# Optimization experiments

Hardware: AMD Instinct MI355X
Metric: run time of the kernel (lower is better)

## Reference

```python
import jax, jax.numpy as jnp
import numpy as np

B, T, H, N = 1, 256, 32, 128
HN = H * N
KVH = 8
KV_DIM = KVH * N
KV_REPEAT = HN // KV_DIM
ROPE_THETA = 10000.0
EPS = 1e-6
NTK_ALPHA = 10.0
YARN_MAX = 4096.0
LORA_W, LORA_A, LORA_V, LORA_G = 64, 64, 32, 128
LAYER_ID = 1


def t5_rmsnorm(x, w):
    xf = x.astype(jnp.float32)
    var = jnp.mean(xf * xf, axis=-1, keepdims=True)
    return (w * (xf * jax.lax.rsqrt(var + EPS))).astype(x.dtype)


def rotate_half(x):
    h = x.shape[-1] // 2
    return jnp.concatenate([-x[..., h:], x[..., :h]], axis=-1)


def rope_cache(cache_pos, seq_len, rotary_dim):
    # YaRN-style mix of short/long inv_freq, per compute_rope_cache_range
    half = rotary_dim // 2
    fs = jnp.arange(half, dtype=jnp.float32)
    inv_short = 1.0 / ROPE_THETA ** (fs / half)
    inv_long = 1.0 / (ROPE_THETA * NTK_ALPHA ** (fs / half))
    pos = cache_pos.astype(jnp.float32) + jnp.arange(seq_len, dtype=jnp.float32)[None, :]  # [B,T]
    mix = jnp.clip(pos / YARN_MAX, 0.0, 1.0)[..., None]
    freqs = (1.0 - mix) * (pos[..., None] * inv_short) + mix * (pos[..., None] * inv_long)
    emb = jnp.concatenate([freqs, freqs], axis=-1)  # [B,T,rotary_dim]
    return jnp.cos(emb), jnp.sin(emb)


def _forward(x_in, v_first, state, cache_position, w0, w1, w2, a0, a1, a2, v0, v1, v2, g1, g2,
             r_k, R_, K_, V_, O_, R_bias, K_bias, V_bias, ln_r, ln_k, ln1, ln2):
    x = t5_rmsnorm(x_in, ln1)  # [B,T,HN]
    # float path of fpx_matmul: x @ W.T (+ bias), i.e. the dequantized math
    r = x @ R_.T + R_bias
    k = x @ K_.T + K_bias
    v = x @ V_.T + V_bias
    r = t5_rmsnorm(r.reshape(B, T, H, N), ln_r)      # [B,T,H,N]
    k = t5_rmsnorm(k.reshape(B, T, KVH, N), ln_k)    # [B,T,KVH,N]
    cos, sin = rope_cache(cache_position, T, N)      # [B,T,N]
    cos_, sin_ = cos[:, :, None, :], sin[:, :, None, :]
    r = r * cos_ + rotate_half(r) * sin_
    k = k * cos_ + rotate_half(k) * sin_
    # decay lora: w = -softplus(-(tanh(x@w1)@w2 + w0)) - 0.5
    w = jnp.tanh(x @ w1) @ w2 + w0
    w = -jax.nn.softplus(-w) - 0.5
    # GQA repeat_kv: each kv head repeated KV_REPEAT times contiguously
    v = v.reshape(B, T, KVH, N)
    k = jnp.repeat(k, KV_REPEAT, axis=2).reshape(B, T, HN)
    v = jnp.repeat(v, KV_REPEAT, axis=2).reshape(B, T, HN)
    a = jax.nn.sigmoid((x @ a1) @ a2 + a0)
    g = jax.nn.sigmoid(x @ g1) @ g2
    k4 = k.reshape(B, T, H, N)
    kk = (k4 / jnp.maximum(jnp.linalg.norm(k4, axis=-1, keepdims=True), 1e-12)).reshape(B, T, HN)
    k = k * (1.0 - w + a)
    aa = -kk
    bb = kk * a
    if LAYER_ID == 0:
        v_first = v
    else:
        gate = jax.nn.sigmoid((x @ v1) @ v2 + v0)
        v = v + (v_first - v) * gate
    w = -jnp.exp(w.astype(jnp.float32))  # log-decay for the recurrence

    def to_tm(t):  # [B,T,HN] or [B,T,H,N] -> time-major [T,B,H,N]
        return jnp.moveaxis(t.reshape(B, T, H, N), 1, 0)

    rt, wt, kt, vt, at, bt = map(to_tm, (r, w, k, v, aa, bb))

    def step(S, inp):
        # RWKV-7: S = S*diag(exp(w)) + S @ (a b^T) + v k^T ; out = S @ r
        r_t, w_t, k_t, v_t, a_t, b_t = inp
        sa = jnp.einsum('bhij,bhj->bhi', S, a_t)
        S = S * jnp.exp(w_t)[:, :, None, :] + sa[..., None] * b_t[:, :, None, :] + v_t[..., None] * k_t[:, :, None, :]
        return S, jnp.einsum('bhij,bhj->bhi', S, r_t)

    S_final, outs = jax.lax.scan(step, state.astype(jnp.float32), (rt, wt, kt, vt, at, bt))
    xx = jnp.moveaxis(outs, 0, 1).reshape(B, T, HN) * (float(N) ** -0.5)
    bonus = jnp.sum(r.reshape(B, T, H, N) * k.reshape(B, T, H, N) * r_k, axis=-1, keepdims=True) * v.reshape(B, T, H, N)
    xx = xx.astype(r.dtype) + bonus.reshape(B, T, HN)
    x_res = x_in + (xx * g) @ O_.T
    out = t5_rmsnorm(x_res, ln2)
    return out, x[:, -1], S_final, v_first, x_res


def setup_inputs() -> dict:
    key = jax.random.key(0)
    ks = iter(jax.random.split(key, 32))
    rn = lambda *s: jax.random.normal(next(ks), s, dtype=jnp.float32)
    wt = lambda *s: rn(*s) * 0.02
    return dict(
        x_in=rn(B, T, HN),
        v_first=rn(B, T, HN),
        state=jnp.zeros((B, H, N, N), jnp.float32),
        cache_position=jnp.zeros((B, 1), jnp.int32),
        w0=wt(HN), w1=wt(HN, LORA_W), w2=wt(LORA_W, HN),
        a0=wt(HN), a1=wt(HN, LORA_A), a2=wt(LORA_A, HN),
        v0=wt(HN), v1=wt(HN, LORA_V), v2=wt(LORA_V, HN),
        g1=wt(HN, LORA_G), g2=wt(LORA_G, HN),
        r_k=wt(H, N),
        R_=wt(HN, HN), K_=wt(KV_DIM, HN), V_=wt(KV_DIM, HN), O_=wt(HN, HN),
        R_bias=wt(HN), K_bias=wt(KV_DIM), V_bias=wt(KV_DIM),
        ln_r=jnp.ones((N,), jnp.float32), ln_k=jnp.ones((N,), jnp.float32),
        ln1=jnp.ones((HN,), jnp.float32), ln2=jnp.ones((HN,), jnp.float32),
    )


def reference(x_in, v_first, state, cache_position, w0, w1, w2, a0, a1, a2, v0, v1, v2, g1, g2,
              r_k, R_, K_, V_, O_, R_bias, K_bias, V_bias, ln_r, ln_k, ln1, ln2):
    return _forward(x_in, v_first, state, cache_position, w0, w1, w2, a0, a1, a2, v0, v1, v2,
                    g1, g2, r_k, R_, K_, V_, O_, R_bias, K_bias, V_bias, ln_r, ln_k, ln1, ln2)
```

## Files before the change

kernel.cpp:

```cpp
#include <hip/hip_runtime.h>
#include <cstdint>
#include <cstddef>

#define T_ 256
#define HN_ 4096
#define H_ 32
#define N_ 128
#define SR_ 6464

typedef __attribute__((ext_vector_type(8))) short short8;
typedef __attribute__((ext_vector_type(4))) float f32x4;

__device__ __forceinline__ short f2bf(float f) {
    uint32_t u = __builtin_bit_cast(uint32_t, f);
    u = (u + 0x7fffu + ((u >> 16) & 1u)) >> 16;
    return (short)u;
}
__device__ __forceinline__ short f2bfc(float f) {
    return (short)((__builtin_bit_cast(uint32_t, f) + 0x8000u) >> 16);
}
__device__ __forceinline__ short8 cvt8r(float4 lo, float4 hi) {
    short8 v;
    v[0] = f2bfc(lo.x); v[1] = f2bfc(lo.y); v[2] = f2bfc(lo.z); v[3] = f2bfc(lo.w);
    v[4] = f2bfc(hi.x); v[5] = f2bfc(hi.y); v[6] = f2bfc(hi.z); v[7] = f2bfc(hi.w);
    return v;
}
__device__ __forceinline__ f32x4 mfma16(short8 a, short8 b, f32x4 c) {
    return __builtin_amdgcn_mfma_f32_16x16x32_bf16(a, b, c, 0, 0, 0);
}
__device__ __forceinline__ float sigm(float x) { return 1.f / (1.f + expf(-x)); }
__device__ __forceinline__ float splus(float x) { return (x > 20.f) ? x : log1pf(expf(x)); }

__device__ __forceinline__ float bf1(ushort u) {
    return __builtin_bit_cast(float, (uint32_t)u << 16);
}
__device__ __forceinline__ void gload_lds16(const void* g, void* l) {
    __builtin_amdgcn_global_load_lds(
        (const __attribute__((address_space(1))) void*)g,
        (__attribute__((address_space(3))) void*)l, 16, 0, 0);
}

template <int CTRL>
__device__ __forceinline__ float dpp_add(float v) {
    int p = __builtin_amdgcn_mov_dpp(__builtin_bit_cast(int, v), CTRL, 0xF, 0xF, true);
    return v + __builtin_bit_cast(float, p);
}
__device__ __forceinline__ float reduce64(float v) {
    v = dpp_add<0xB1>(v);
    v = dpp_add<0x4E>(v);
    v = dpp_add<0x124>(v);
    v = dpp_add<0x128>(v);
    v = dpp_add<0x142>(v);
    v = dpp_add<0x143>(v);
    int r = __builtin_amdgcn_readlane(__builtin_bit_cast(int, v), 63);
    return __builtin_bit_cast(float, r);
}

__device__ __forceinline__ void gemm_core(
    const ushort* __restrict__ A, const float* __restrict__ Brow,
    int kbeg, float* LB, f32x4 acc[2][2]) {
    const int tid = threadIdx.x, wid = tid >> 6, l = tid & 63;
    const int ar = l & 15, ak = (l >> 4) * 8;
    const int mBase = wid * 32;

    const int p1 = tid, p2 = tid + 512;
    const int r1 = p1 >> 5, c1 = (p1 & 31) ^ (r1 & 7);
    const int r2 = p2 >> 5, c2 = (p2 & 31) ^ (r2 & 7);
    const float* sb1 = Brow + (size_t)r1 * 4096 + kbeg + c1 * 4;
    const float* sb2 = Brow + (size_t)r2 * 4096 + kbeg + c2 * 4;
    float* d1 = LB + wid * 256;
    float* d2 = LB + 2048 + wid * 256;

    const ushort* pa0 = A + (size_t)(mBase + ar) * 4096 + kbeg + ak;
    const ushort* pa1 = pa0 + (size_t)16 * 4096;

    const int rb0 = ar * 128, rb1 = (16 + ar) * 128;
    const int sx = ar & 7;
    const int cb = (l >> 4) * 2;

    short8 Ae[8], Ao[8];

#define STAGEB(s, rb) { \
    gload_lds16(sb1 + (size_t)(s) * 128, d1 + (rb) * 4096); \
    gload_lds16(sb2 + (size_t)(s) * 128, d2 + (rb) * 4096); }

#define LA(B_, s) { \
    B_[0] = *(const short8*)(pa0 + (size_t)(s) * 128);      \
    B_[1] = *(const short8*)(pa1 + (size_t)(s) * 128);      \
    B_[2] = *(const short8*)(pa0 + (size_t)(s) * 128 + 32); \
    B_[3] = *(const short8*)(pa1 + (size_t)(s) * 128 + 32); \
    B_[4] = *(const short8*)(pa0 + (size_t)(s) * 128 + 64); \
    B_[5] = *(const short8*)(pa1 + (size_t)(s) * 128 + 64); \
    B_[6] = *(const short8*)(pa0 + (size_t)(s) * 128 + 96); \
    B_[7] = *(const short8*)(pa1 + (size_t)(s) * 128 + 96); }

#define CKK(kk, B_, Lb_) { \
    const int cc = (kk) * 8 + cb; \
    float4 l0 = *(const float4*)(Lb_ + rb0 + ((cc ^ sx) * 4)); \
    float4 h0 = *(const float4*)(Lb_ + rb0 + (((cc + 1) ^ sx) * 4)); \
    float4 l1 = *(const float4*)(Lb_ + rb1 + ((cc ^ sx) * 4)); \
    float4 h1 = *(const float4*)(Lb_ + rb1 + (((cc + 1) ^ sx) * 4)); \
    short8 b0 = cvt8r(l0, h0), b1 = cvt8r(l1, h1); \
    acc[0][0] = mfma16(B_[2 * (kk)], b0, acc[0][0]); \
    acc[0][1] = mfma16(B_[2 * (kk)], b1, acc[0][1]); \
    acc[1][0] = mfma16(B_[2 * (kk) + 1], b0, acc[1][0]); \
    acc[1][1] = mfma16(B_[2 * (kk) + 1], b1, acc[1][1]); }

#define COMPUTE(rb, B_) { const float* Lb_ = LB + (rb) * 4096; \
    CKK(0, B_, Lb_) CKK(1, B_, Lb_) CKK(2, B_, Lb_) CKK(3, B_, Lb_) }

    STAGEB(0, 0)
    LA(Ae, 0)
    STAGEB(1, 1)

    for (int su = 0; su < 4; su++) {
        const int s0 = su * 2, s1 = su * 2 + 1;
        LA(Ao, (s0 + 1 < 8) ? s0 + 1 : 7)
        STAGEB((s0 + 2 < 8) ? s0 + 2 : 7, (s0 + 2) % 3)
        asm volatile("s_waitcnt vmcnt(12)" ::: "memory");
        __builtin_amdgcn_s_barrier();
        __builtin_amdgcn_sched_barrier(0);
        COMPUTE(s0 % 3, Ae)
        __builtin_amdgcn_s_barrier();

        LA(Ae, (s1 + 1 < 8) ? s1 + 1 : 7)
        STAGEB((s1 + 2 < 8) ? s1 + 2 : 7, (s1 + 2) % 3)
        asm volatile("s_waitcnt vmcnt(12)" ::: "memory");
        __builtin_amdgcn_s_barrier();
        __builtin_amdgcn_sched_barrier(0);
        COMPUTE(s1 % 3, Ao)
        __builtin_amdgcn_s_barrier();
    }
    asm volatile("s_waitcnt vmcnt(0)" ::: "memory");
#undef STAGEB
#undef LA
#undef CKK
#undef COMPUTE
}

__global__ __launch_bounds__(256) void rmsnorm_k(const float* __restrict__ in,
                                                 const float* __restrict__ w,
                                                 float* __restrict__ outF,
                                                 ushort* __restrict__ outB,
                                                 float* __restrict__ lastrow) {
    int t = blockIdx.x, tid = threadIdx.x;
    const float4* in4 = (const float4*)(in + (size_t)t * HN_);
    const float4* w4 = (const float4*)w;
    float4 v[4]; float ss = 0.f;
#pragma unroll
    for (int q = 0; q < 4; q++) {
        v[q] = in4[q * 256 + tid];
        ss += v[q].x * v[q].x + v[q].y * v[q].y + v[q].z * v[q].z + v[q].w * v[q].w;
    }
#pragma unroll
    for (int o = 32; o; o >>= 1) ss += __shfl_down(ss, o);
    __shared__ float red[4];
    if ((tid & 63) == 0) red[tid >> 6] = ss;
    __syncthreads();
    float tot = red[0] + red[1] + red[2] + red[3];
    float sc = rsqrtf(tot * (1.f / HN_) + 1e-6f);
#pragma unroll
    for (int q = 0; q < 4; q++) {
        float4 wv = w4[q * 256 + tid];
        float4 r;
        r.x = wv.x * v[q].x * sc; r.y = wv.y * v[q].y * sc;
        r.z = wv.z * v[q].z * sc; r.w = wv.w * v[q].w * sc;
        int idx = q * 256 + tid;
        if (outF) ((float4*)(outF + (size_t)t * HN_))[idx] = r;
        if (outB) {
            ushort4 b;
            b.x = (ushort)f2bf(r.x); b.y = (ushort)f2bf(r.y);
            b.z = (ushort)f2bf(r.z); b.w = (ushort)f2bf(r.w);
            ((ushort4*)(outB + (size_t)t * HN_))[idx] = b;
        }
        if (lastrow && t == T_ - 1) ((float4*)lastrow)[idx] = r;
    }
}

__global__ __launch_bounds__(512, 2) void gemm_rkvt(
    const ushort* __restrict__ A,
    const float* __restrict__ Rw, const float* __restrict__ Kw,
    const float* __restrict__ Vw, const float* __restrict__ WT,
    float* __restrict__ COMB) {
    __shared__ __align__(16) float LB[12288];
    const int tid = threadIdx.x, wid = tid >> 6, l = tid & 63;
    const int mBase = wid * 32;
    const int nB = blockIdx.x * 32;
    const int kbeg = blockIdx.y * 1024;

    const float* Bp; int brow;
    if (nB < 4096)      { Bp = Rw; brow = nB; }
    else if (nB < 5120) { Bp = Kw; brow = nB - 4096; }
    else if (nB < 6144) { Bp = Vw; brow = nB - 5120; }
    else                { Bp = WT; brow = nB - 6144; }

    f32x4 acc[2][2];
#pragma unroll
    for (int i = 0; i < 2; i++)
#pragma unroll
        for (int j = 0; j < 2; j++) acc[i][j] = f32x4{0.f, 0.f, 0.f, 0.f};

    gemm_core(A, Bp + (size_t)brow * 4096, kbeg, LB, acc);

    const int rl = (l >> 4) * 4, cl = l & 15;
#pragma unroll
    for (int mf = 0; mf < 2; mf++)
#pragma unroll
        for (int nf = 0; nf < 2; nf++)
#pragma unroll
            for (int e = 0; e < 4; e++)
                unsafeAtomicAdd(&COMB[(size_t)(mBase + mf * 16 + rl + e) * SR_ + nB + nf * 16 + cl],
                                acc[mf][nf][e]);
}

__global__ __launch_bounds__(512, 2) void gemm_o(
    const ushort* __restrict__ A,
    const float* __restrict__ B,
    float* __restrict__ C) {
    __shared__ __align__(16) float LB[12288];
    const int tid = threadIdx.x, wid = tid >> 6, l = tid & 63;
    const int mBase = wid * 32;
    const int nB = blockIdx.x * 32;
    const int kbeg = blockIdx.y * 1024;

    f32x4 acc[2][2];
#pragma unroll
    for (int i = 0; i < 2; i++)
#pragma unroll
        for (int j = 0; j < 2; j++) acc[i][j] = f32x4{0.f, 0.f, 0.f, 0.f};

    gemm_core(A, B + (size_t)nB * 4096, kbeg, LB, acc);

    const int rl = (l >> 4) * 4, cl = l & 15;
#pragma unroll
    for (int mf = 0; mf < 2; mf++)
#pragma unroll
        for (int nf = 0; nf < 2; nf++)
#pragma unroll
            for (int e = 0; e < 4; e++)
                unsafeAtomicAdd(&C[(size_t)(mBase + mf * 16 + rl + e) * 4096 + nB + nf * 16 + cl],
                                acc[mf][nf][e]);
}

__global__ __launch_bounds__(512) void gemm_s2(
    const ushort* __restrict__ TCB,
    const float* __restrict__ w2, const float* __restrict__ a2,
    const float* __restrict__ v2, const float* __restrict__ g2,
    const float* __restrict__ w0, const float* __restrict__ a0,
    const float* __restrict__ v0,
    float* __restrict__ WPRE, float* __restrict__ APRE,
    float* __restrict__ VGPRE, float* __restrict__ GARR) {
    const int z = blockIdx.y;
    int Aoff, K; const float* B; const float* bias; float* out;
    if (z == 0)      { Aoff = 0;   K = 64;  B = w2; bias = w0;      out = WPRE; }
    else if (z == 1) { Aoff = 64;  K = 64;  B = a2; bias = a0;      out = APRE; }
    else if (z == 2) { Aoff = 128; K = 32;  B = v2; bias = v0;      out = VGPRE; }
    else             { Aoff = 160; K = 128; B = g2; bias = nullptr; out = GARR; }

    const int tid = threadIdx.x, wid = tid >> 6, l = tid & 63;
    const int ar = l & 15, ak = (l >> 4) * 8;
    const int mBase = wid * 32;
    const int nB = blockIdx.x * 32;

    f32x4 acc[2][2];
#pragma unroll
    for (int i = 0; i < 2; i++)
#pragma unroll
        for (int j = 0; j < 2; j++) acc[i][j] = f32x4{0.f, 0.f, 0.f, 0.f};

    for (int k0 = 0; k0 < K; k0 += 32) {
        const ushort* pA = TCB + (size_t)(mBase + ar) * 320 + Aoff + k0 + ak;
        short8 av0 = *(const short8*)pA;
        short8 av1 = *(const short8*)(pA + (size_t)16 * 320);
        short8 bv0, bv1;
#pragma unroll
        for (int e = 0; e < 8; e++) {
            bv0[e] = f2bfc(B[(size_t)(k0 + ak + e) * 4096 + nB + ar]);
            bv1[e] = f2bfc(B[(size_t)(k0 + ak + e) * 4096 + nB + 16 + ar]);
        }
        acc[0][0] = mfma16(av0, bv0, acc[0][0]);
        acc[0][1] = mfma16(av0, bv1, acc[0][1]);
        acc[1][0] = mfma16(av1, bv0, acc[1][0]);
        acc[1][1] = mfma16(av1, bv1, acc[1][1]);
    }
    const int rl = (l >> 4) * 4, cl = l & 15;
#pragma unroll
    for (int mf = 0; mf < 2; mf++)
#pragma unroll
        for (int nf = 0; nf < 2; nf++) {
            int col = nB + nf * 16 + cl;
            float bv = bias ? bias[col] : 0.f;
#pragma unroll
            for (int e = 0; e < 4; e++)
                out[(size_t)(mBase + mf * 16 + rl + e) * 4096 + col] = acc[mf][nf][e] + bv;
        }
}

__global__ __launch_bounds__(256) void wcat2_k(const float* __restrict__ w1p,
                                               const float* __restrict__ a1p,
                                               const float* __restrict__ v1p,
                                               const float* __restrict__ g1p,
                                               float* __restrict__ WT) {
    const int kb = blockIdx.x * 64, tile = blockIdx.y;
    const float* src; int ldw, jo, nb, W;
    if (tile == 0)      { src = w1p; ldw = 64;  jo = 0;  nb = 0;   W = 64; }
    else if (tile == 1) { src = a1p; ldw = 64;  jo = 0;  nb = 64;  W = 64; }
    else if (tile == 2) { src = v1p; ldw = 32;  jo = 0;  nb = 128; W = 32; }
    else if (tile == 3) { src = g1p; ldw = 128; jo = 0;  nb = 160; W = 64; }
    else                { src = g1p; ldw = 128; jo = 64; nb = 224; W = 64; }
    __shared__ float lds[64][65];
    const int ti = threadIdx.x & 63, wi = threadIdx.x >> 6;
    if (ti < W)
        for (int i = wi; i < 64; i += 4)
            lds[i][ti] = src[(size_t)(kb + i) * ldw + jo + ti];
    __syncthreads();
    for (int i2 = wi; i2 < W; i2 += 4)
        WT[(size_t)(nb + i2) * 4096 + kb + ti] = lds[ti][i2];
}

__global__ __launch_bounds__(256) void init_comb_k(const float* __restrict__ Rb,
                                                   const float* __restrict__ Kb,
                                                   const float* __restrict__ Vb,
                                                   float* __restrict__ COMB) {
    int t = blockIdx.x;
    for (int c = threadIdx.x; c < SR_; c += 256) {
        float b = (c < 4096) ? Rb[c] : (c < 5120) ? Kb[c - 4096]
                : (c < 6144) ? Vb[c - 5120] : 0.f;
        COMB[(size_t)t * SR_ + c] = b;
    }
}

__global__ __launch_bounds__(256) void act_k(const float* __restrict__ COMB,
                                             ushort* __restrict__ TCB) {
    int idx = blockIdx.x * 256 + threadIdx.x;
    if (idx >= 256 * 288) return;
    int t = idx / 288, c = idx % 288;
    float v = COMB[(size_t)t * SR_ + 6144 + c];
    if (c < 64) v = tanhf(v);
    else if (c >= 160) v = sigm(v);
    TCB[t * 320 + c] = (ushort)f2bf(v);
}

__global__ __launch_bounds__(256) void prep_k(
    const float* __restrict__ COMB, const float* __restrict__ wpre,
    const float* __restrict__ apre, const float* __restrict__ vgpre,
    const float* __restrict__ vfirst, const float* __restrict__ garr,
    const float* __restrict__ rkg, const int* __restrict__ cpos,
    const float* __restrict__ lnr, const float* __restrict__ lnk,
    ushort* __restrict__ SFB) {
    const int tp = blockIdx.x, hg = blockIdx.y;
    const int tid = threadIdx.x;
    const int w = tid >> 6, lane = tid & 63;
    const int t0 = tp * 2, t1 = t0 + 1;

    float e = (float)lane * (1.f / 64.f);
    float inv_s = exp2f(-13.287712379549449f * e);
    float inv_l = exp2f(-13.287712379549449f - 3.321928094887362f * e);
    float base = (float)cpos[0];
    float pos0 = base + (float)t0, pos1 = base + (float)t1;
    float mix0 = fminf(fmaxf(pos0 * (1.f / 4096.f), 0.f), 1.f);
    float mix1 = fminf(fmaxf(pos1 * (1.f / 4096.f), 0.f), 1.f);
    float fr0 = pos0 * ((1.f - mix0) * inv_s + mix0 * inv_l);
    float fr1 = pos1 * ((1.f - mix1) * inv_s + mix1 * inv_l);
    float cA = cosf(fr0), sA = sinf(fr0);
    float cB = cosf(fr1), sB = sinf(fr1);

    float lr0 = lnr[lane], lr1 = lnr[lane + 64];
    float lk0 = lnk[lane], lk1 = lnk[lane + 64];

    for (int hb = hg * 4; hb < hg * 4 + 4; hb++) {
        int h = hb * 4 + w;
        int kv = h >> 2;
        float rk0 = rkg[h * 128 + lane], rk1 = rkg[h * 128 + 64 + lane];

        auto STEPQ = [&](int t, float cc, float ss,
                         float& Rr0, float& Rr1, float& Kf0, float& Kf1,
                         float& Aa0, float& Aa1, float& Bb0, float& Bb1,
                         float& Dd0, float& Dd1, float& Vv0, float& Vv1,
                         float& Gg0, float& Gg1) {
            size_t tS = (size_t)t * SR_;
            float r0 = COMB[tS + h * 128 + lane];
            float r1 = COMB[tS + h * 128 + 64 + lane];
            float sm = reduce64(r0 * r0 + r1 * r1);
            float sc = rsqrtf(sm * (1.f / 128.f) + 1e-6f);
            float rn0 = lr0 * r0 * sc, rn1 = lr1 * r1 * sc;
            Rr0 = rn0 * cc - rn1 * ss; Rr1 = rn1 * cc + rn0 * ss;
            float k0 = COMB[tS + 4096 + kv * 128 + lane];
            float k1 = COMB[tS + 4096 + kv * 128 + 64 + lane];
            float ks = reduce64(k0 * k0 + k1 * k1);
            float ksc = rsqrtf(ks * (1.f / 128.f) + 1e-6f);
            float kn0 = lk0 * k0 * ksc, kn1 = lk1 * k1 * ksc;
            float kr0 = kn0 * cc - kn1 * ss, kr1 = kn1 * cc + kn0 * ss;
            float nr = reduce64(kr0 * kr0 + kr1 * kr1);
            float inv = 1.f / fmaxf(sqrtf(nr), 1e-12f);
            float kk0 = kr0 * inv, kk1 = kr1 * inv;
            int ch0 = h * 128 + lane, ch1 = ch0 + 64;
            size_t tb = (size_t)t * HN_;
            float wv0 = -splus(-wpre[tb + ch0]) - 0.5f;
            float wv1 = -splus(-wpre[tb + ch1]) - 0.5f;
            Dd0 = expf(-expf(wv0)); Dd1 = expf(-expf(wv1));
            float av0 = sigm(apre[tb + ch0]);
            float av1 = sigm(apre[tb + ch1]);
            float vg0 = sigm(vgpre[tb + ch0]);
            float vg1 = sigm(vgpre[tb + ch1]);
            float vr0 = COMB[tS + 5120 + kv * 128 + lane];
            float vr1 = COMB[tS + 5120 + kv * 128 + 64 + lane];
            Vv0 = vr0 + (vfirst[tb + ch0] - vr0) * vg0;
            Vv1 = vr1 + (vfirst[tb + ch1] - vr1) * vg1;
            Kf0 = kr0 * (1.f - wv0 + av0); Kf1 = kr1 * (1.f - wv1 + av1);
            Aa0 = -kk0; Aa1 = -kk1;
            Bb0 = kk0 * av0; Bb1 = kk1 * av1;
            Gg0 = garr[tb + ch0]; Gg1 = garr[tb + ch1];
        };

        float r00, r01, k00, k01, a00, a01, b00, b01, d00, d01, v00, v01, g00, g01;
        float r10, r11, k10, k11, a10, a11, b10, b11, d10, d11, v10, v11, g10, g11;
        STEPQ(t0, cA, sA, r00, r01, k00, k01, a00, a01, b00, b01, d00, d01, v00, v01, g00, g01);
        STEPQ(t1, cB, sB, r10, r11, k10, k11, a10, a11, b10, b11, d10, d11, v10, v11, g10, g11);

        float* rf = (float*)(SFB + ((size_t)h * 128 + tp) * 3072);
        rf[0    + lane] = a00;        rf[0    + 64 + lane] = a01;
        rf[128  + lane] = d00 * a10;  rf[128  + 64 + lane] = d01 * a11;
        rf[256  + lane] = d00 * r00;  rf[256  + 64 + lane] = d01 * r01;
        rf[384  + lane] = r10;        rf[384  + 64 + lane] = r11;
        rf[512  + lane] = d00 * d10;  rf[512  + 64 + lane] = d01 * d11;
        rf[640  + lane] = b00 * d10;  rf[640  + 64 + lane] = b01 * d11;
        rf[768  + lane] = k00 * d10;  rf[768  + 64 + lane] = k01 * d11;
        rf[896  + lane] = b10;        rf[896  + 64 + lane] = b11;
        rf[1024 + lane] = k10;        rf[1024 + 64 + lane] = k11;
        ushort* us = (ushort*)rf;
        us[2304 + lane] = (ushort)f2bf(v00); us[2304 + 64 + lane] = (ushort)f2bf(v01);
        us[2432 + lane] = (ushort)f2bf(v10); us[2432 + 64 + lane] = (ushort)f2bf(v11);
        us[2560 + lane] = (ushort)f2bf(g00); us[2560 + 64 + lane] = (ushort)f2bf(g01);
        us[2688 + lane] = (ushort)f2bf(g10); us[2688 + 64 + lane] = (ushort)f2bf(g11);

        float C1  = reduce64(b00 * a10 + b01 * a11);
        float C2  = reduce64(k00 * a10 + k01 * a11);
        float C3  = reduce64(b00 * r00 + b01 * r01);
        float C4  = reduce64(k00 * r00 + k01 * r01);
        float BD0 = reduce64(r00 * k00 * rk0 + r01 * k01 * rk1);
        float BD1 = reduce64(r10 * k10 * rk0 + r11 * k11 * rk1);
        if (lane == 0) {
            rf[1408] = C1; rf[1409] = C2; rf[1410] = C3;
            rf[1411] = C4; rf[1412] = BD0; rf[1413] = BD1;
        }
    }
}

#define SDP_ 5
#define SNBP_ 6
__global__ __launch_bounds__(256) void scan_k(
    const float* __restrict__ state_in,
    const ushort* __restrict__ SFB,
    ushort* __restrict__ yb, float* __restrict__ Sout,
    ushort* __restrict__ dummy) {
    const int h = blockIdx.x, sp = blockIdx.y;
    const int tid = threadIdx.x;
    const int wv = tid >> 6, ln = tid & 63;
    const int i = sp * 4 + wv;
    const int j0 = ln * 2;

    float S0, S1;
    {
        float2 s2 = *(const float2*)(state_in + ((size_t)h * 128 + i) * 128 + j0);
        S0 = s2.x; S1 = s2.y;
    }

    __shared__ __align__(16) ushort lds_s[SNBP_][3072];
    const ushort* hbase = SFB + (size_t)h * 128 * 3072;

    auto STAGE = [&](int buf, int tp) {
        if (wv < 3) {
            const ushort* src = hbase + (size_t)(tp & 127) * 3072 + wv * 1024 + ln * 8;
            gload_lds16(src,       &lds_s[buf][wv * 1024]);
            gload_lds16(src + 512, &lds_s[buf][wv * 1024 + 512]);
        }
    };

#pragma unroll
    for (int d = 0; d < SDP_; d++) STAGE(d, d);

    float pend_y0 = 0.f, pend_y1 = 0.f;
    float r1c0 = 0.f, r1c1 = 0.f, bd1c = 0.f, vi1c = 0.f, gi1c = 0.f;
    for (int Io = 0; Io < 132; Io += 6) {
#pragma unroll
        for (int u = 0; u < 6; u++) {
            const int I = Io + u;
            if (I >= 128) break;
            const int bc = u;
            const int bs = (u + SDP_) % 6;

            if (wv < 3) {
                if (I < SDP_) asm volatile("s_waitcnt vmcnt(8)" ::: "memory");
                else          asm volatile("s_waitcnt vmcnt(16)" ::: "memory");
            }
            __builtin_amdgcn_s_barrier();
            __builtin_amdgcn_sched_barrier(0);
            asm volatile("" ::: "memory");

            if (ln == 0) {
                ushort* p0 = (I >= 1) ? (yb + (size_t)(2 * I - 2) * HN_ + h * 128 + i)
                                      : (dummy + tid);
                *p0 = (ushort)f2bf(pend_y0);
                ushort* p1 = (I >= 2) ? (yb + (size_t)(2 * I - 3) * HN_ + h * 128 + i)
                                      : (dummy + 256 + tid);
                *p1 = (ushort)f2bf(pend_y1);
            }

            STAGE(bs, I + SDP_);

            const ushort* L = lds_s[bc];
            const float* Lf = (const float*)L;
            float2 A0 = *(const float2*)(Lf + 0    + j0);
            float2 WA = *(const float2*)(Lf + 128  + j0);
            float2 WR = *(const float2*)(Lf + 256  + j0);
            float2 R1 = *(const float2*)(Lf + 384  + j0);
            float2 W2 = *(const float2*)(Lf + 512  + j0);
            float2 BW = *(const float2*)(Lf + 640  + j0);
            float2 KW = *(const float2*)(Lf + 768  + j0);
            float2 B1 = *(const float2*)(Lf + 896  + j0);
            float2 K1 = *(const float2*)(Lf + 1024 + j0);
            float vi0 = bf1(L[2304 + i]);
            float vi1 = bf1(L[2432 + i]);
            float gi0 = bf1(L[2560 + i]);
            float gi1 = bf1(L[2688 + i]);
            const float* Sc = Lf + 1408;
            float c1 = Sc[0], c2 = Sc[1], c3 = Sc[2], c4 = Sc[3];
            float bd0 = Sc[4], bd1 = Sc[5];

            float up = fmaf(S0, A0.x, S1 * A0.y);
            float pp = fmaf(S0, WA.x, S1 * WA.y);
            float yp = fmaf(S0, WR.x, S1 * WR.y);
            float op = fmaf(S0, r1c0, S1 * r1c1);
            float u_   = reduce64(up);
            float p_   = reduce64(pp);
            float yb0  = reduce64(yp);
            float od1  = reduce64(op);

            pend_y1 = fmaf(od1, 0.08838834764831845f, bd1c * vi1c) * gi1c;

            float sa0 = u_;
            float sa1 = fmaf(sa0, c1, fmaf(vi0, c2, p_));
            float od0 = fmaf(sa0, c3, fmaf(vi0, c4, yb0));
            pend_y0 = fmaf(od0, 0.08838834764831845f, bd0 * vi0) * gi0;

            S0 = fmaf(sa0, BW.x, S0 * W2.x);
            S0 = fmaf(vi0, KW.x, S0);
            S0 = fmaf(sa1, B1.x, S0);
            S0 = fmaf(vi1, K1.x, S0);
            S1 = fmaf(sa0, BW.y, S1 * W2.y);
            S1 = fmaf(vi0, KW.y, S1);
            S1 = fmaf(sa1, B1.y, S1);
            S1 = fmaf(vi1, K1.y, S1);

            r1c0 = R1.x; r1c1 = R1.y;
            bd1c = bd1; vi1c = vi1; gi1c = gi1;
        }
    }

    {
        float op = fmaf(S0, r1c0, S1 * r1c1);
        float od1 = reduce64(op);
        float cp1 = fmaf(od1, 0.08838834764831845f, bd1c * vi1c) * gi1c;
        if (ln == 0) {
            yb[(size_t)255 * HN_ + h * 128 + i] = (ushort)f2bf(cp1);
            yb[(size_t)254 * HN_ + h * 128 + i] = (ushort)f2bf(pend_y0);
            yb[(size_t)253 * HN_ + h * 128 + i] = (ushort)f2bf(pend_y1);
        }
    }

    float* pS = Sout + ((size_t)h * 128 + i) * 128 + j0;
    *(float2*)pS = make_float2(S0, S1);
}

extern "C" void kernel_launch(void* const* d_in, const int* in_sizes, int n_in,
                              void* d_out, int out_size, void* d_ws, size_t ws_size,
                              hipStream_t stream) {
    const float* x_in   = (const float*)d_in[0];
    const float* vfirst = (const float*)d_in[1];
    const float* state  = (const float*)d_in[2];
    const int*   cpos   = (const int*)d_in[3];
    const float* w0 = (const float*)d_in[4];
    const float* w1 = (const float*)d_in[5];
    const float* w2 = (const float*)d_in[6];
    const float* a0 = (const float*)d_in[7];
    const float* a1 = (const float*)d_in[8];
    const float* a2 = (const float*)d_in[9];
    const float* v0 = (const float*)d_in[10];
    const float* v1 = (const float*)d_in[11];
    const float* v2 = (const float*)d_in[12];
    const float* g1 = (const float*)d_in[13];
    const float* g2 = (const float*)d_in[14];
    const float* r_k = (const float*)d_in[15];
    const float* R_ = (const float*)d_in[16];
    const float* K_ = (const float*)d_in[17];
    const float* V_ = (const float*)d_in[18];
    const float* O_ = (const float*)d_in[19];
    const float* Rb = (const float*)d_in[20];
    const float* Kb = (const float*)d_in[21];
    const float* Vb = (const float*)d_in[22];
    const float* ln_r = (const float*)d_in[23];
    const float* ln_k = (const float*)d_in[24];
    const float* ln1 = (const float*)d_in[25];
    const float* ln2 = (const float*)d_in[26];

    float* ws = (float*)d_ws;
    constexpr size_t OFF_XB   = 0;
    constexpr size_t OFF_COMB = 524288;
    constexpr size_t OFF_WT   = 2179072;
    constexpr size_t OFF_TCB  = 3489792;
    constexpr size_t OFF_WPRE = 3530752;
    constexpr size_t OFF_APRE = 4579328;
    constexpr size_t OFF_VGPRE= 5627904;
    constexpr size_t OFF_G    = 6676480;
    constexpr size_t OFF_SF   = 7757824;
    constexpr size_t OFF_DUM  = 14049280;
    constexpr size_t OFF_YB   = OFF_XB;

    ushort* XB  = (ushort*)(ws + OFF_XB);
    float* COMB = ws + OFF_COMB;
    float* WT   = ws + OFF_WT;
    ushort* TCB = (ushort*)(ws + OFF_TCB);
    float* WPRE = ws + OFF_WPRE;
    float* APRE = ws + OFF_APRE;
    float* VGPRE= ws + OFF_VGPRE;
    float* GARR = ws + OFF_G;
    ushort* SFB = (ushort*)(ws + OFF_SF);
    ushort* DUM = (ushort*)(ws + OFF_DUM);
    ushort* YB  = (ushort*)(ws + OFF_YB);

    float* out = (float*)d_out;
    float* out0  = out;
    float* xlast = out + 1048576;
    float* Sfin  = out + 1052672;
    float* vfout = out + 1576960;
    float* xres  = out + 2625536;

    hipMemcpyAsync(vfout, vfirst, (size_t)1048576 * 4, hipMemcpyDeviceToDevice, stream);
    hipMemcpyAsync(xres, x_in, (size_t)1048576 * 4, hipMemcpyDeviceToDevice, stream);

    rmsnorm_k<<<T_, 256, 0, stream>>>(x_in, ln1, nullptr, XB, xlast);

    wcat2_k<<<dim3(64, 5), 256, 0, stream>>>(w1, a1, v1, g1, WT);
    hipMemsetAsync(WT + (size_t)288 * 4096, 0, (size_t)32 * 4096 * 4, stream);
    init_comb_k<<<T_, 256, 0, stream>>>(Rb, Kb, Vb, COMB);

    gemm_rkvt<<<dim3(202, 4), 512, 0, stream>>>(XB, R_, K_, V_, WT, COMB);

    act_k<<<288, 256, 0, stream>>>(COMB, TCB);

    gemm_s2<<<dim3(128, 4), 512, 0, stream>>>(TCB, w2, a2, v2, g2, w0, a0, v0,
                                              WPRE, APRE, VGPRE, GARR);

    prep_k<<<dim3(128, 2), 256, 0, stream>>>(COMB, WPRE, APRE, VGPRE, vfirst, GARR,
                                             r_k, cpos, ln_r, ln_k, SFB);

    scan_k<<<dim3(32, 32), 256, 0, stream>>>(state, SFB, YB, Sfin, DUM);

    gemm_o<<<dim3(128, 4), 512, 0, stream>>>(YB, O_, xres);

    rmsnorm_k<<<T_, 256, 0, stream>>>(xres, ln2, out0, nullptr, nullptr);
}
```

Before: 308.5 us.

## Stage GEMM B tile through registers and store it as bf16 in LDS

The shared GEMM core previously copied fp32 weight tiles straight from global memory into a triple-buffered LDS area. Every wave then reread the fp32 values and converted them to bf16 before each MFMA, so all eight waves repeated the same conversions. Now each thread loads its slice of the B tile into registers, converts it to bf16 once, and writes it into a double-buffered bf16 LDS area. This cuts LDS from 48KB to 16KB, halves LDS read traffic and removes the redundant conversions. In exchange it loses the asynchronous global-to-LDS copy, adds register pressure for the staged values, and drops the trailing barrier in each step, relying on the next step's barrier for ordering.

```diff
diff --git a/kernel.cpp b/kernel.cpp
--- a/kernel.cpp
+++ b/kernel.cpp
@@ -58,31 +58,29 @@
 
 __device__ __forceinline__ void gemm_core(
     const ushort* __restrict__ A, const float* __restrict__ Brow,
-    int kbeg, float* LB, f32x4 acc[2][2]) {
+    int kbeg, ushort* LH, f32x4 acc[2][2]) {
     const int tid = threadIdx.x, wid = tid >> 6, l = tid & 63;
     const int ar = l & 15, ak = (l >> 4) * 8;
     const int mBase = wid * 32;
 
-    const int p1 = tid, p2 = tid + 512;
-    const int r1 = p1 >> 5, c1 = (p1 & 31) ^ (r1 & 7);
-    const int r2 = p2 >> 5, c2 = (p2 & 31) ^ (r2 & 7);
-    const float* sb1 = Brow + (size_t)r1 * 4096 + kbeg + c1 * 4;
-    const float* sb2 = Brow + (size_t)r2 * 4096 + kbeg + c2 * 4;
-    float* d1 = LB + wid * 256;
-    float* d2 = LB + 2048 + wid * 256;
+    const int brw = tid >> 4, bc8 = tid & 15;
+    const float* bsrc = Brow + (size_t)brw * 4096 + kbeg + bc8 * 8;
+    const int hoff = brw * 128 + ((bc8 ^ (brw & 7)) * 8);
 
     const ushort* pa0 = A + (size_t)(mBase + ar) * 4096 + kbeg + ak;
     const ushort* pa1 = pa0 + (size_t)16 * 4096;
 
+    const int akc = ak >> 3;
+    const int sx0 = ar & 7;
     const int rb0 = ar * 128, rb1 = (16 + ar) * 128;
-    const int sx = ar & 7;
-    const int cb = (l >> 4) * 2;
 
     short8 Ae[8], Ao[8];
-
-#define STAGEB(s, rb) { \
-    gload_lds16(sb1 + (size_t)(s) * 128, d1 + (rb) * 4096); \
-    gload_lds16(sb2 + (size_t)(s) * 128, d2 + (rb) * 4096); }
+    float4 B0a, B0b, B1a, B1b;
+
+#define LB0(s) { B0a = *(const float4*)(bsrc + (size_t)(s) * 128); \
+                 B0b = *(const float4*)(bsrc + (size_t)(s) * 128 + 4); }
+#define LB1(s) { B1a = *(const float4*)(bsrc + (size_t)(s) * 128); \
+                 B1b = *(const float4*)(bsrc + (size_t)(s) * 128 + 4); }
 
 #define LA(B_, s) { \
     B_[0] = *(const short8*)(pa0 + (size_t)(s) * 128);      \
@@ -94,45 +92,42 @@
     B_[6] = *(const short8*)(pa0 + (size_t)(s) * 128 + 96); \
     B_[7] = *(const short8*)(pa1 + (size_t)(s) * 128 + 96); }
 
-#define CKK(kk, B_, Lb_) { \
-    const int cc = (kk) * 8 + cb; \
-    float4 l0 = *(const float4*)(Lb_ + rb0 + ((cc ^ sx) * 4)); \
-    float4 h0 = *(const float4*)(Lb_ + rb0 + (((cc + 1) ^ sx) * 4)); \
-    float4 l1 = *(const float4*)(Lb_ + rb1 + ((cc ^ sx) * 4)); \
-    float4 h1 = *(const float4*)(Lb_ + rb1 + (((cc + 1) ^ sx) * 4)); \
-    short8 b0 = cvt8r(l0, h0), b1 = cvt8r(l1, h1); \
+#define CKK(kk, B_, Hb_) { \
+    const int sl = ((kk) * 4 + akc) ^ sx0; \
+    short8 b0 = *(const short8*)((Hb_) + rb0 + sl * 8); \
+    short8 b1 = *(const short8*)((Hb_) + rb1 + sl * 8); \
     acc[0][0] = mfma16(B_[2 * (kk)], b0, acc[0][0]); \
     acc[0][1] = mfma16(B_[2 * (kk)], b1, acc[0][1]); \
     acc[1][0] = mfma16(B_[2 * (kk) + 1], b0, acc[1][0]); \
     acc[1][1] = mfma16(B_[2 * (kk) + 1], b1, acc[1][1]); }
 
-#define COMPUTE(rb, B_) { const float* Lb_ = LB + (rb) * 4096; \
-    CKK(0, B_, Lb_) CKK(1, B_, Lb_) CKK(2, B_, Lb_) CKK(3, B_, Lb_) }
-
-    STAGEB(0, 0)
+#define COMPUTE(Hb_, B_) { CKK(0, B_, Hb_) CKK(1, B_, Hb_) CKK(2, B_, Hb_) CKK(3, B_, Hb_) }
+
+    LB0(0)
     LA(Ae, 0)
-    STAGEB(1, 1)
+    LB1(1)
 
     for (int su = 0; su < 4; su++) {
         const int s0 = su * 2, s1 = su * 2 + 1;
-        LA(Ao, (s0 + 1 < 8) ? s0 + 1 : 7)
-        STAGEB((s0 + 2 < 8) ? s0 + 2 : 7, (s0 + 2) % 3)
-        asm volatile("s_waitcnt vmcnt(12)" ::: "memory");
+
+        *(short8*)(LH + hoff) = cvt8r(B0a, B0b);
+        LB0((s0 + 2 < 8) ? s0 + 2 : 7)
+        LA(Ao, s0 + 1)
+        asm volatile("s_waitcnt lgkmcnt(0)" ::: "memory");
         __builtin_amdgcn_s_barrier();
         __builtin_amdgcn_sched_barrier(0);
-        COMPUTE(s0 % 3, Ae)
-        __builtin_amdgcn_s_barrier();
-
+        COMPUTE(LH, Ae)
+
+        *(short8*)(LH + 4096 + hoff) = cvt8r(B1a, B1b);
+        LB1((s1 + 2 < 8) ? s1 + 2 : 7)
         LA(Ae, (s1 + 1 < 8) ? s1 + 1 : 7)
-        STAGEB((s1 + 2 < 8) ? s1 + 2 : 7, (s1 + 2) % 3)
-        asm volatile("s_waitcnt vmcnt(12)" ::: "memory");
+        asm volatile("s_waitcnt lgkmcnt(0)" ::: "memory");
         __builtin_amdgcn_s_barrier();
         __builtin_amdgcn_sched_barrier(0);
-        COMPUTE(s1 % 3, Ao)
-        __builtin_amdgcn_s_barrier();
-    }
-    asm volatile("s_waitcnt vmcnt(0)" ::: "memory");
-#undef STAGEB
+        COMPUTE(LH + 4096, Ao)
+    }
+#undef LB0
+#undef LB1
 #undef LA
 #undef CKK
 #undef COMPUTE
@@ -182,7 +177,7 @@
     const float* __restrict__ Rw, const float* __restrict__ Kw,
     const float* __restrict__ Vw, const float* __restrict__ WT,
     float* __restrict__ COMB) {
-    __shared__ __align__(16) float LB[12288];
+    __shared__ __align__(16) ushort LH[8192];
     const int tid = threadIdx.x, wid = tid >> 6, l = tid & 63;
     const int mBase = wid * 32;
     const int nB = blockIdx.x * 32;
@@ -200,7 +195,7 @@
 #pragma unroll
         for (int j = 0; j < 2; j++) acc[i][j] = f32x4{0.f, 0.f, 0.f, 0.f};
 
-    gemm_core(A, Bp + (size_t)brow * 4096, kbeg, LB, acc);
+    gemm_core(A, Bp + (size_t)brow * 4096, kbeg, LH, acc);
 
     const int rl = (l >> 4) * 4, cl = l & 15;
 #pragma unroll
@@ -217,7 +212,7 @@
     const ushort* __restrict__ A,
     const float* __restrict__ B,
     float* __restrict__ C) {
-    __shared__ __align__(16) float LB[12288];
+    __shared__ __align__(16) ushort LH[8192];
     const int tid = threadIdx.x, wid = tid >> 6, l = tid & 63;
     const int mBase = wid * 32;
     const int nB = blockIdx.x * 32;
@@ -229,7 +224,7 @@
 #pragma unroll
         for (int j = 0; j < 2; j++) acc[i][j] = f32x4{0.f, 0.f, 0.f, 0.f};
 
-    gemm_core(A, B + (size_t)nB * 4096, kbeg, LB, acc);
+    gemm_core(A, B + (size_t)nB * 4096, kbeg, LH, acc);
 
     const int rl = (l >> 4) * 4, cl = l & 15;
 #pragma unroll
```

Measured after the change: 282.9 us. 8.3% less time.
